# Kernel optimization log

Measured on AMD Instinct MI355X. Metric: run time of the kernel, lower is better.

## Reference

```python
import jax, jax.numpy as jnp
import numpy as np

N_ATOMS = 100000
N_EDGES = 1000000
HIDDEN = 64
OUT_DIM = 128
N_LAYERS = 3
N_ELEMENTS = 100


def setup_inputs() -> dict:
    key = jax.random.key(0)
    ks = jax.random.split(key, 14)
    s = 0.05
    return {
        "atomic_numbers": jax.random.randint(ks[0], (N_ATOMS,), 0, N_ELEMENTS),
        "positions": jax.random.normal(ks[1], (N_ATOMS, 3), jnp.float32),
        "lattice": jax.random.normal(ks[2], (3, 3), jnp.float32),
        "edge_index": jax.random.randint(ks[3], (2, N_EDGES), 0, N_ATOMS),
        "emb_table": jax.random.normal(ks[4], (N_ELEMENTS, HIDDEN), jnp.float32) * s,
        "W_lin": jax.random.normal(ks[5], (N_LAYERS, HIDDEN, HIDDEN), jnp.float32) * s,
        "b_lin": jax.random.normal(ks[6], (N_LAYERS, HIDDEN), jnp.float32) * s,
        "W_gate": jax.random.normal(ks[7], (N_LAYERS, 2 * HIDDEN, HIDDEN), jnp.float32) * s,
        "b_gate": jax.random.normal(ks[8], (N_LAYERS, HIDDEN), jnp.float32) * s,
        "W_out1": jax.random.normal(ks[9], (HIDDEN, HIDDEN), jnp.float32) * s,
        "b_out1": jax.random.normal(ks[10], (HIDDEN,), jnp.float32) * s,
        "W_out2": jax.random.normal(ks[11], (HIDDEN, OUT_DIM), jnp.float32) * s,
        "b_out2": jax.random.normal(ks[12], (OUT_DIM,), jnp.float32) * s,
    }


def reference(atomic_numbers, positions, lattice, edge_index,
              emb_table, W_lin, b_lin, W_gate, b_gate,
              W_out1, b_out1, W_out2, b_out2):
    # positions/lattice unused when edge_index is provided (matches original).
    x = emb_table[atomic_numbers]            # [N, H] embedding lookup
    row, col = edge_index[0], edge_index[1]
    n = x.shape[0]
    for i in range(W_lin.shape[0]):          # fixed small layer count
        xn = x[col]                          # [E, H] neighbor gather
        gate_in = jnp.concatenate([x[row], xn], axis=-1)  # [E, 2H]
        gate = jax.nn.sigmoid(gate_in @ W_gate[i] + b_gate[i])
        messages = gate * (xn @ W_lin[i] + b_lin[i])       # [E, H]
        agg = jax.ops.segment_sum(messages, row, num_segments=n)  # scatter-add
        x = jax.nn.relu(agg + x @ W_lin[i] + b_lin[i])
    pooled = x.mean(axis=0)                  # [H] mean pool over atoms
    h = jax.nn.relu(pooled @ W_out1 + b_out1)
    return h @ W_out2 + b_out2               # [OUT_DIM]
```

## Files before the change

### kernel.cpp

```cpp
#include <hip/hip_runtime.h>
#include <hip/hip_bf16.h>
#include <stdint.h>


#define H 64
#define BSHIFT 7
#define BROWS 128
#define NLOG2E -1.4426950408889634f

typedef __attribute__((ext_vector_type(8))) short bf16x8;
typedef __attribute__((ext_vector_type(4))) float f32x4;

__device__ __forceinline__ ushort f2bf(float f) {
  uint32_t u = __float_as_uint(f);
  u = (u + 0x7fffu + ((u >> 16) & 1u)) >> 16;
  return (ushort)u;
}
__device__ __forceinline__ uint32_t pack_gl(float gc, float lin) {
  uint32_t ug = __float_as_uint(gc);
  ug = (ug + 0x7fffu + ((ug >> 16) & 1u)) >> 16;
  uint32_t ul = __float_as_uint(lin);
  ul = ((ul + 0x7fffu + ((ul >> 16) & 1u)) >> 16) << 16;
  return ul | ug;
}
__device__ __forceinline__ float unpack_gc(uint32_t p) {
  return __uint_as_float(p << 16);
}
__device__ __forceinline__ float unpack_lin(uint32_t p) {
  return __uint_as_float(p & 0xffff0000u);
}
__device__ __forceinline__ float sig_from_neglog2(float arg) {
  return __builtin_amdgcn_rcpf(1.f + exp2f(arg));
}

__global__ __launch_bounds__(256) void prep_kernel(
    const float* __restrict__ Wl, const float* __restrict__ Wg,
    const float* __restrict__ bg, bf16x8* __restrict__ wprep,
    float* __restrict__ bgs) {
  const int t = blockIdx.x * 256 + threadIdx.x;
  if (t < 192) bgs[t] = bg[t] * NLOG2E;
  if (t >= 4608) return;
  const int l = t / 1536;
  const int rem = t - l * 1536;
  const int mat = rem >> 9;
  const int rem2 = rem & 511;
  const int nt = rem2 >> 7;
  const int ks = (rem2 >> 6) & 1;
  const int lane = rem2 & 63;
  const int kg = lane >> 4, l15 = lane & 15;
  const float* src;
  float s;
  if (mat == 0)      { src = Wl + (size_t)l * 4096;        s = 1.f; }
  else if (mat == 1) { src = Wg + (size_t)l * 8192;        s = NLOG2E; }
  else               { src = Wg + (size_t)l * 8192 + 4096; s = NLOG2E; }
  bf16x8 v;
#pragma unroll
  for (int j = 0; j < 8; j++)
    v[j] = (short)f2bf(src[(size_t)(ks * 32 + kg * 8 + j) * 64 + nt * 16 + l15] * s);
  wprep[t] = v;
}

__global__ __launch_bounds__(256) void bucket_hist_kernel(
    const int* __restrict__ row, int* __restrict__ bcnt, int E, int nbuck) {
  __shared__ int cnt[1024];
  const int tid = threadIdx.x;
  for (int b = tid; b < nbuck; b += 256) cnt[b] = 0;
  __syncthreads();
  for (int e = blockIdx.x * blockDim.x + tid; e < E; e += gridDim.x * blockDim.x)
    atomicAdd(&cnt[row[e] >> BSHIFT], 1);
  __syncthreads();
  for (int b = tid; b < nbuck; b += 256)
    if (cnt[b]) atomicAdd(&bcnt[b], cnt[b]);
}

__global__ __launch_bounds__(1024) void bucket_scan_kernel(
    const int* __restrict__ bcnt, int* __restrict__ bstart,
    int* __restrict__ bcur, int* __restrict__ offs, float* __restrict__ pool,
    int nbuck, int N, int E) {
  __shared__ int sh[1024];
  const int tid = threadIdx.x;
  if (tid < 64) pool[tid] = 0.f;
  const int mine = (tid < nbuck) ? bcnt[tid] : 0;
  sh[tid] = mine;
  __syncthreads();
  for (int off = 1; off < 1024; off <<= 1) {
    const int v = (tid >= off) ? sh[tid - off] : 0;
    __syncthreads();
    sh[tid] += v;
    __syncthreads();
  }
  if (tid < nbuck) {
    const int ex = sh[tid] - mine;
    bstart[tid] = ex;
    bcur[tid] = ex;
  }
  if (tid == 0) {
    bstart[nbuck] = E;
    offs[N] = E;
  }
}

#define SCHUNK 4096
__global__ __launch_bounds__(256) void bucket_scatter_kernel(
    const int* __restrict__ row, const int* __restrict__ col,
    int* __restrict__ bcur, uint2* __restrict__ ebuf, int E, int nbuck) {
  __shared__ int cnt[1024], base[1024];
  const int tid = threadIdx.x;
  const int start = blockIdx.x * SCHUNK;
  const int end = min(start + SCHUNK, E);
  for (int b = tid; b < nbuck; b += 256) cnt[b] = 0;
  __syncthreads();
  for (int e = start + tid; e < end; e += 256)
    atomicAdd(&cnt[row[e] >> BSHIFT], 1);
  __syncthreads();
  for (int b = tid; b < nbuck; b += 256) {
    if (cnt[b]) base[b] = atomicAdd(&bcur[b], cnt[b]);
    cnt[b] = 0;
  }
  __syncthreads();
  for (int e = start + tid; e < end; e += 256) {
    const int r = row[e];
    const int b = r >> BSHIFT;
    const int pos = base[b] + atomicAdd(&cnt[b], 1);
    ebuf[pos] = make_uint2((uint32_t)r, (uint32_t)col[e]);
  }
}

__global__ __launch_bounds__(256) void csr_build_kernel(
    const uint2* __restrict__ ebuf, const int* __restrict__ bstart,
    int* __restrict__ offs, int* __restrict__ cols, int N) {
  __shared__ int cnt[BROWS], sc[BROWS];
  const int tid = threadIdx.x;
  const int b = blockIdx.x;
  const int bs = bstart[b], be = bstart[b + 1];
  const int rowbase = b << BSHIFT;
  if (tid < BROWS) cnt[tid] = 0;
  __syncthreads();
  for (int e = bs + tid; e < be; e += 256)
    atomicAdd(&cnt[ebuf[e].x & (BROWS - 1)], 1);
  __syncthreads();
  if (tid < BROWS) sc[tid] = cnt[tid];
  __syncthreads();
  for (int off = 1; off < BROWS; off <<= 1) {
    const int v = (tid >= off && tid < BROWS) ? sc[tid - off] : 0;
    __syncthreads();
    if (tid < BROWS) sc[tid] += v;
    __syncthreads();
  }
  if (tid < BROWS) {
    sc[tid] -= cnt[tid];
    cnt[tid] = 0;
    const int r = rowbase + tid;
    if (r < N) offs[r] = bs + sc[tid];
  }
  __syncthreads();
  for (int e = bs + tid; e < be; e += 256) {
    const uint2 u = ebuf[e];
    const int rl = u.x & (BROWS - 1);
    const int pos = sc[rl] + atomicAdd(&cnt[rl], 1);
    cols[bs + pos] = (int)u.y;
  }
}

template <bool FIRST>
__global__ __launch_bounds__(256) void node_mm3_mfma(
    const ushort* __restrict__ x, const int* __restrict__ an,
    const float* __restrict__ emb, const bf16x8* __restrict__ wp,
    const float* __restrict__ bl, const float* __restrict__ bgs,
    float* __restrict__ gr, uint32_t* __restrict__ glpk, int N) {
  const int tid = threadIdx.x;
  const int lane = tid & 63, wid = tid >> 6;
  const int l15 = lane & 15, kg = lane >> 4;

  bf16x8 bfrag[3][4][2];
#pragma unroll
  for (int mat = 0; mat < 3; mat++)
#pragma unroll
    for (int nt = 0; nt < 4; nt++)
#pragma unroll
      for (int ks = 0; ks < 2; ks++)
        bfrag[mat][nt][ks] = wp[(((mat * 4 + nt) * 2 + ks) << 6) + lane];

  const int mbase = blockIdx.x * 64 + wid * 16;
  const int arow = mbase + l15;
  const int arow_c = min(arow, N - 1);

  bf16x8 afrag0, afrag1;
  if (FIRST) {
    const int a = an[arow_c];
    const float* src = emb + (size_t)a * H + kg * 8;
    const float4 u0 = *(const float4*)(src);
    const float4 u1 = *(const float4*)(src + 4);
    const float4 u2 = *(const float4*)(src + 32);
    const float4 u3 = *(const float4*)(src + 36);
    bf16x8 t0, t1;
    t0[0] = (short)f2bf(u0.x); t0[1] = (short)f2bf(u0.y);
    t0[2] = (short)f2bf(u0.z); t0[3] = (short)f2bf(u0.w);
    t0[4] = (short)f2bf(u1.x); t0[5] = (short)f2bf(u1.y);
    t0[6] = (short)f2bf(u1.z); t0[7] = (short)f2bf(u1.w);
    t1[0] = (short)f2bf(u2.x); t1[1] = (short)f2bf(u2.y);
    t1[2] = (short)f2bf(u2.z); t1[3] = (short)f2bf(u2.w);
    t1[4] = (short)f2bf(u3.x); t1[5] = (short)f2bf(u3.y);
    t1[6] = (short)f2bf(u3.z); t1[7] = (short)f2bf(u3.w);
    afrag0 = t0; afrag1 = t1;
  } else {
    const ushort* src = x + (size_t)arow_c * H + kg * 8;
    afrag0 = *(const bf16x8*)(src);
    afrag1 = *(const bf16x8*)(src + 32);
  }

  f32x4 accL[4], accR[4], accC[4];
#pragma unroll
  for (int nt = 0; nt < 4; nt++) {
    const float blv = bl[nt * 16 + l15];
    const float bgv = bgs[nt * 16 + l15];
    accL[nt] = (f32x4){blv, blv, blv, blv};
    accR[nt] = (f32x4){0.f, 0.f, 0.f, 0.f};
    accC[nt] = (f32x4){bgv, bgv, bgv, bgv};
  }
#pragma unroll
  for (int nt = 0; nt < 4; nt++) {
    accL[nt] = __builtin_amdgcn_mfma_f32_16x16x32_bf16(afrag0, bfrag[0][nt][0], accL[nt], 0, 0, 0);
    accL[nt] = __builtin_amdgcn_mfma_f32_16x16x32_bf16(afrag1, bfrag[0][nt][1], accL[nt], 0, 0, 0);
    accR[nt] = __builtin_amdgcn_mfma_f32_16x16x32_bf16(afrag0, bfrag[1][nt][0], accR[nt], 0, 0, 0);
    accR[nt] = __builtin_amdgcn_mfma_f32_16x16x32_bf16(afrag1, bfrag[1][nt][1], accR[nt], 0, 0, 0);
    accC[nt] = __builtin_amdgcn_mfma_f32_16x16x32_bf16(afrag0, bfrag[2][nt][0], accC[nt], 0, 0, 0);
    accC[nt] = __builtin_amdgcn_mfma_f32_16x16x32_bf16(afrag1, bfrag[2][nt][1], accC[nt], 0, 0, 0);
  }
#pragma unroll
  for (int nt = 0; nt < 4; nt++) {
#pragma unroll
    for (int r = 0; r < 4; r++) {
      const int atom = mbase + kg * 4 + r;
      if (atom < N) {
        const size_t o = (size_t)atom * H + nt * 16 + l15;
        gr[o] = accR[nt][r];
        glpk[o] = pack_gl(accC[nt][r], accL[nt][r]);
      }
    }
  }
}

__global__ __launch_bounds__(256) void agg_kernel(
    const float* __restrict__ gr, const uint32_t* __restrict__ glpk,
    const int* __restrict__ offs, const int* __restrict__ cols,
    ushort* __restrict__ x, int N) {
  const int lane = threadIdx.x & 63, w = threadIdx.x >> 6;
  for (int i = blockIdx.x * 4 + w; i < N; i += gridDim.x * 4) {
    const int s = offs[i], e = offs[i + 1];
    const float gri = gr[(size_t)i * H + lane];
    float acc = 0.f;
    for (int cb = s; cb < e; cb += 64) {
      const int nchunk = min(64, e - cb);
      const int myc = (lane < nchunk) ? cols[cb + lane] : 0;
      int j = 0;
      for (; j + 7 < nchunk; j += 8) {
        uint32_t p[8];
#pragma unroll
        for (int q = 0; q < 8; q++) {
          const int c = __shfl(myc, j + q);
          p[q] = glpk[(size_t)c * H + lane];
        }
#pragma unroll
        for (int q = 0; q < 8; q++)
          acc += unpack_lin(p[q]) * sig_from_neglog2(gri + unpack_gc(p[q]));
      }
      for (; j < nchunk; j++) {
        const int c = __shfl(myc, j);
        const uint32_t p0 = glpk[(size_t)c * H + lane];
        acc += unpack_lin(p0) * sig_from_neglog2(gri + unpack_gc(p0));
      }
    }
    const float li = unpack_lin(glpk[(size_t)i * H + lane]);
    x[(size_t)i * H + lane] = f2bf(fmaxf(acc + li, 0.f));
  }
}

__global__ void pool_kernel(const ushort* __restrict__ x,
                            float* __restrict__ pool, int N) {
  __shared__ float ps[4][64];
  const int tid = threadIdx.x, c = tid & 63, wid = tid >> 6;
  float s = 0.f;
  for (int i = blockIdx.x * 4 + wid; i < N; i += gridDim.x * 4)
    s += __uint_as_float(((uint32_t)x[(size_t)i * H + c]) << 16);
  ps[wid][c] = s;
  __syncthreads();
  if (tid < 64) {
    const float t = ps[0][tid] + ps[1][tid] + ps[2][tid] + ps[3][tid];
    atomicAdd(&pool[tid], t);
  }
}

__global__ void mlp_kernel(const float* __restrict__ pool,
                           const float* __restrict__ W1,
                           const float* __restrict__ b1,
                           const float* __restrict__ W2,
                           const float* __restrict__ b2,
                           float* __restrict__ out, float invN) {
  __shared__ float p[64], h[64];
  const int tid = threadIdx.x;
  if (tid < 64) p[tid] = pool[tid] * invN;
  __syncthreads();
  if (tid < 64) {
    float s = b1[tid];
    for (int k = 0; k < 64; k++) s = fmaf(p[k], W1[k * 64 + tid], s);
    h[tid] = fmaxf(s, 0.f);
  }
  __syncthreads();
  float s = b2[tid];
  for (int k = 0; k < 64; k++) s = fmaf(h[k], W2[k * 128 + tid], s);
  out[tid] = s;
}

extern "C" void kernel_launch(void* const* d_in, const int* in_sizes, int n_in,
                              void* d_out, int out_size, void* d_ws,
                              size_t ws_size, hipStream_t stream) {
  const int*   an  = (const int*)d_in[0];
  const int*   ei  = (const int*)d_in[3];
  const float* emb = (const float*)d_in[4];
  const float* Wl  = (const float*)d_in[5];
  const float* bl  = (const float*)d_in[6];
  const float* Wg  = (const float*)d_in[7];
  const float* bg  = (const float*)d_in[8];
  const float* W1  = (const float*)d_in[9];
  const float* b1  = (const float*)d_in[10];
  const float* W2  = (const float*)d_in[11];
  const float* b2  = (const float*)d_in[12];
  float* out = (float*)d_out;

  const int N = in_sizes[0];
  const int E = in_sizes[3] / 2;
  const int* row = ei;
  const int* col = ei + E;
  const int nbuck = (N + BROWS - 1) >> BSHIFT;

  const size_t NH = (size_t)N * H;
  char* ws = (char*)d_ws;
  ushort*   x    = (ushort*)(ws);
  float*    gr   = (float*)(ws + NH * 2);
  uint32_t* glpk = (uint32_t*)(ws + NH * 2 + NH * 4);
  char* p = ws + NH * 2 + NH * 4 + NH * 4;
  int*    offs   = (int*)p;    p += ((size_t)N + 1) * 4;
  int*    cols   = (int*)p;    p += (size_t)E * 4;
  int*    bcnt   = (int*)p;    p += 4096;
  int*    bstart = (int*)p;    p += 4100;
  int*    bcur   = (int*)p;    p += 4096;
  uint2*  ebuf   = (uint2*)p;  p += (size_t)E * 8;
  bf16x8* wprep  = (bf16x8*)p; p += 4608 * 16;
  float*  bgs    = (float*)p;  p += 192 * 4;
  float*  pool   = (float*)p;

  prep_kernel<<<18, 256, 0, stream>>>(Wl, Wg, bg, wprep, bgs);

  hipMemsetAsync(bcnt, 0, (size_t)nbuck * 4, stream);
  bucket_hist_kernel<<<1024, 256, 0, stream>>>(row, bcnt, E, nbuck);
  bucket_scan_kernel<<<1, 1024, 0, stream>>>(bcnt, bstart, bcur, offs, pool,
                                             nbuck, N, E);
  bucket_scatter_kernel<<<(E + SCHUNK - 1) / SCHUNK, 256, 0, stream>>>(
      row, col, bcur, ebuf, E, nbuck);
  csr_build_kernel<<<nbuck, 256, 0, stream>>>(ebuf, bstart, offs, cols, N);

  const int mmGrid = (N + 63) / 64;
  const int aggGrid = (N + 3) / 4;
  for (int l = 0; l < 3; l++) {
    const bf16x8* wp  = wprep + (size_t)l * 1536;
    const float*  bll = bl + (size_t)l * H;
    const float*  bgl = bgs + (size_t)l * H;
    if (l == 0)
      node_mm3_mfma<true><<<mmGrid, 256, 0, stream>>>(x, an, emb, wp, bll, bgl,
                                                      gr, glpk, N);
    else
      node_mm3_mfma<false><<<mmGrid, 256, 0, stream>>>(x, an, emb, wp, bll, bgl,
                                                       gr, glpk, N);
    agg_kernel<<<aggGrid, 256, 0, stream>>>(gr, glpk, offs, cols, x, N);
  }

  pool_kernel<<<1024, 256, 0, stream>>>(x, pool, N);
  mlp_kernel<<<1, 128, 0, stream>>>(pool, W1, b1, W2, b2, out, 1.0f / (float)N);
}
```

Before: 400.9 us.

## Replace CSR build with bucketed LDS-atomic aggregation and fuse pooling

Drops the per-row CSR construction kernel and aggregates messages directly over 64-row edge buckets, accumulating into shared memory with atomics. Edge records are packed into 32 bits (local row plus column), gr is stored in bf16, and mean pooling is fused into the final aggregation layer. This cuts a kernel launch, one edge pass and memory traffic, in exchange for LDS atomic contention and extra rounding of the gate term.

```diff
diff --git a/kernel.cpp b/kernel.cpp
--- a/kernel.cpp
+++ b/kernel.cpp
@@ -4,8 +4,8 @@
 
 
 #define H 64
-#define BSHIFT 7
-#define BROWS 128
+#define BSHIFT 6
+#define BROWS 64
 #define NLOG2E -1.4426950408889634f
 
 typedef __attribute__((ext_vector_type(8))) short bf16x8;
@@ -62,7 +62,7 @@
 
 __global__ __launch_bounds__(256) void bucket_hist_kernel(
     const int* __restrict__ row, int* __restrict__ bcnt, int E, int nbuck) {
-  __shared__ int cnt[1024];
+  __shared__ int cnt[2048];
   const int tid = threadIdx.x;
   for (int b = tid; b < nbuck; b += 256) cnt[b] = 0;
   __syncthreads();
@@ -75,13 +75,15 @@
 
 __global__ __launch_bounds__(1024) void bucket_scan_kernel(
     const int* __restrict__ bcnt, int* __restrict__ bstart,
-    int* __restrict__ bcur, int* __restrict__ offs, float* __restrict__ pool,
-    int nbuck, int N, int E) {
+    int* __restrict__ bcur, float* __restrict__ pool, int nbuck, int E) {
   __shared__ int sh[1024];
   const int tid = threadIdx.x;
   if (tid < 64) pool[tid] = 0.f;
-  const int mine = (tid < nbuck) ? bcnt[tid] : 0;
-  sh[tid] = mine;
+  const int i0 = 2 * tid, i1 = 2 * tid + 1;
+  const int v0 = (i0 < nbuck) ? bcnt[i0] : 0;
+  const int v1 = (i1 < nbuck) ? bcnt[i1] : 0;
+  const int s = v0 + v1;
+  sh[tid] = s;
   __syncthreads();
   for (int off = 1; off < 1024; off <<= 1) {
     const int v = (tid >= off) ? sh[tid - off] : 0;
@@ -89,22 +91,17 @@
     sh[tid] += v;
     __syncthreads();
   }
-  if (tid < nbuck) {
-    const int ex = sh[tid] - mine;
-    bstart[tid] = ex;
-    bcur[tid] = ex;
-  }
-  if (tid == 0) {
-    bstart[nbuck] = E;
-    offs[N] = E;
-  }
+  const int ex = sh[tid] - s;
+  if (i0 < nbuck) { bstart[i0] = ex;      bcur[i0] = ex; }
+  if (i1 < nbuck) { bstart[i1] = ex + v0; bcur[i1] = ex + v0; }
+  if (tid == 0) bstart[nbuck] = E;
 }
 
 #define SCHUNK 4096
 __global__ __launch_bounds__(256) void bucket_scatter_kernel(
     const int* __restrict__ row, const int* __restrict__ col,
-    int* __restrict__ bcur, uint2* __restrict__ ebuf, int E, int nbuck) {
-  __shared__ int cnt[1024], base[1024];
+    int* __restrict__ bcur, uint32_t* __restrict__ ebuf, int E, int nbuck) {
+  __shared__ int cnt[2048], base[2048];
   const int tid = threadIdx.x;
   const int start = blockIdx.x * SCHUNK;
   const int end = min(start + SCHUNK, E);
@@ -122,43 +119,7 @@
     const int r = row[e];
     const int b = r >> BSHIFT;
     const int pos = base[b] + atomicAdd(&cnt[b], 1);
-    ebuf[pos] = make_uint2((uint32_t)r, (uint32_t)col[e]);
-  }
-}
-
-__global__ __launch_bounds__(256) void csr_build_kernel(
-    const uint2* __restrict__ ebuf, const int* __restrict__ bstart,
-    int* __restrict__ offs, int* __restrict__ cols, int N) {
-  __shared__ int cnt[BROWS], sc[BROWS];
-  const int tid = threadIdx.x;
-  const int b = blockIdx.x;
-  const int bs = bstart[b], be = bstart[b + 1];
-  const int rowbase = b << BSHIFT;
-  if (tid < BROWS) cnt[tid] = 0;
-  __syncthreads();
-  for (int e = bs + tid; e < be; e += 256)
-    atomicAdd(&cnt[ebuf[e].x & (BROWS - 1)], 1);
-  __syncthreads();
-  if (tid < BROWS) sc[tid] = cnt[tid];
-  __syncthreads();
-  for (int off = 1; off < BROWS; off <<= 1) {
-    const int v = (tid >= off && tid < BROWS) ? sc[tid - off] : 0;
-    __syncthreads();
-    if (tid < BROWS) sc[tid] += v;
-    __syncthreads();
-  }
-  if (tid < BROWS) {
-    sc[tid] -= cnt[tid];
-    cnt[tid] = 0;
-    const int r = rowbase + tid;
-    if (r < N) offs[r] = bs + sc[tid];
-  }
-  __syncthreads();
-  for (int e = bs + tid; e < be; e += 256) {
-    const uint2 u = ebuf[e];
-    const int rl = u.x & (BROWS - 1);
-    const int pos = sc[rl] + atomicAdd(&cnt[rl], 1);
-    cols[bs + pos] = (int)u.y;
+    ebuf[pos] = ((uint32_t)(r & (BROWS - 1)) << 26) | (uint32_t)col[e];
   }
 }
 
@@ -167,7 +128,7 @@
     const ushort* __restrict__ x, const int* __restrict__ an,
     const float* __restrict__ emb, const bf16x8* __restrict__ wp,
     const float* __restrict__ bl, const float* __restrict__ bgs,
-    float* __restrict__ gr, uint32_t* __restrict__ glpk, int N) {
+    ushort* __restrict__ gr, uint32_t* __restrict__ glpk, int N) {
   const int tid = threadIdx.x;
   const int lane = tid & 63, wid = tid >> 6;
   const int l15 = lane & 15, kg = lane >> 4;
@@ -234,60 +195,88 @@
       const int atom = mbase + kg * 4 + r;
       if (atom < N) {
         const size_t o = (size_t)atom * H + nt * 16 + l15;
-        gr[o] = accR[nt][r];
+        gr[o] = f2bf(accR[nt][r]);
         glpk[o] = pack_gl(accC[nt][r], accL[nt][r]);
       }
     }
   }
 }
 
-__global__ __launch_bounds__(256) void agg_kernel(
-    const float* __restrict__ gr, const uint32_t* __restrict__ glpk,
-    const int* __restrict__ offs, const int* __restrict__ cols,
-    ushort* __restrict__ x, int N) {
-  const int lane = threadIdx.x & 63, w = threadIdx.x >> 6;
-  for (int i = blockIdx.x * 4 + w; i < N; i += gridDim.x * 4) {
-    const int s = offs[i], e = offs[i + 1];
-    const float gri = gr[(size_t)i * H + lane];
-    float acc = 0.f;
-    for (int cb = s; cb < e; cb += 64) {
-      const int nchunk = min(64, e - cb);
-      const int myc = (lane < nchunk) ? cols[cb + lane] : 0;
-      int j = 0;
-      for (; j + 7 < nchunk; j += 8) {
-        uint32_t p[8];
-#pragma unroll
-        for (int q = 0; q < 8; q++) {
-          const int c = __shfl(myc, j + q);
-          p[q] = glpk[(size_t)c * H + lane];
-        }
-#pragma unroll
-        for (int q = 0; q < 8; q++)
-          acc += unpack_lin(p[q]) * sig_from_neglog2(gri + unpack_gc(p[q]));
-      }
-      for (; j < nchunk; j++) {
-        const int c = __shfl(myc, j);
-        const uint32_t p0 = glpk[(size_t)c * H + lane];
-        acc += unpack_lin(p0) * sig_from_neglog2(gri + unpack_gc(p0));
+template <bool LAST>
+__global__ __launch_bounds__(256) void agg_bucket_kernel(
+    const ushort* __restrict__ gr, const uint32_t* __restrict__ glpk,
+    const uint32_t* __restrict__ ebuf, const int* __restrict__ bstart,
+    ushort* __restrict__ x, float* __restrict__ pool, int N) {
+  __shared__ float acc[BROWS * H];
+  __shared__ ushort grs[BROWS * H];
+  __shared__ float pacc[H];
+  const int tid = threadIdx.x;
+  const int lane = tid & 63, w = tid >> 6;
+  const int b = blockIdx.x;
+  const int rowbase = b << BSHIFT;
+
+  {
+    const uint4* gsrc = (const uint4*)(gr + (size_t)rowbase * H);
+    uint4* gdst = (uint4*)grs;
+    gdst[tid] = gsrc[tid];
+    gdst[tid + 256] = gsrc[tid + 256];
+    float4* az = (float4*)acc;
+#pragma unroll
+    for (int q = 0; q < 4; q++) az[tid + q * 256] = make_float4(0.f, 0.f, 0.f, 0.f);
+    if (LAST && tid < 64) pacc[tid] = 0.f;
+  }
+  __syncthreads();
+
+  const int bs = bstart[b], be = bstart[b + 1];
+  for (int cb = bs + w * 64; cb < be; cb += 256) {
+    const int nchunk = min(64, be - cb);
+    const uint32_t mye = (lane < nchunk) ? ebuf[cb + lane] : 0;
+    int j = 0;
+    for (; j + 3 < nchunk; j += 4) {
+      const uint32_t e0 = __shfl(mye, j + 0), e1 = __shfl(mye, j + 1);
+      const uint32_t e2 = __shfl(mye, j + 2), e3 = __shfl(mye, j + 3);
+      const uint32_t p0 = glpk[((e0 & 0x3FFFFFFu) << 6) | lane];
+      const uint32_t p1 = glpk[((e1 & 0x3FFFFFFu) << 6) | lane];
+      const uint32_t p2 = glpk[((e2 & 0x3FFFFFFu) << 6) | lane];
+      const uint32_t p3 = glpk[((e3 & 0x3FFFFFFu) << 6) | lane];
+#pragma unroll
+      for (int q = 0; q < 4; q++) {
+        const uint32_t e = (q == 0) ? e0 : (q == 1) ? e1 : (q == 2) ? e2 : e3;
+        const uint32_t p = (q == 0) ? p0 : (q == 1) ? p1 : (q == 2) ? p2 : p3;
+        const int rl = (int)(e >> 26);
+        const float g = __uint_as_float((uint32_t)grs[(rl << 6) | lane] << 16);
+        const float m = unpack_lin(p) * sig_from_neglog2(g + unpack_gc(p));
+        atomicAdd(&acc[(rl << 6) | lane], m);
       }
     }
-    const float li = unpack_lin(glpk[(size_t)i * H + lane]);
-    x[(size_t)i * H + lane] = f2bf(fmaxf(acc + li, 0.f));
-  }
-}
-
-__global__ void pool_kernel(const ushort* __restrict__ x,
-                            float* __restrict__ pool, int N) {
-  __shared__ float ps[4][64];
-  const int tid = threadIdx.x, c = tid & 63, wid = tid >> 6;
-  float s = 0.f;
-  for (int i = blockIdx.x * 4 + wid; i < N; i += gridDim.x * 4)
-    s += __uint_as_float(((uint32_t)x[(size_t)i * H + c]) << 16);
-  ps[wid][c] = s;
-  __syncthreads();
-  if (tid < 64) {
-    const float t = ps[0][tid] + ps[1][tid] + ps[2][tid] + ps[3][tid];
-    atomicAdd(&pool[tid], t);
+    for (; j < nchunk; j++) {
+      const uint32_t e = __shfl(mye, j);
+      const uint32_t p = glpk[((e & 0x3FFFFFFu) << 6) | lane];
+      const int rl = (int)(e >> 26);
+      const float g = __uint_as_float((uint32_t)grs[(rl << 6) | lane] << 16);
+      const float m = unpack_lin(p) * sig_from_neglog2(g + unpack_gc(p));
+      atomicAdd(&acc[(rl << 6) | lane], m);
+    }
+  }
+  __syncthreads();
+
+  float psum = 0.f;
+#pragma unroll
+  for (int k = 0; k < 16; k++) {
+    const int r = w * 16 + k;
+    const int atom = rowbase + r;
+    if (atom < N) {
+      const float li = unpack_lin(glpk[((size_t)atom << 6) | lane]);
+      float v = acc[(r << 6) | lane] + li;
+      v = fmaxf(v, 0.f);
+      x[((size_t)atom << 6) | lane] = f2bf(v);
+      if (LAST) psum += v;
+    }
+  }
+  if (LAST) {
+    atomicAdd(&pacc[lane], psum);
+    __syncthreads();
+    if (tid < 64) atomicAdd(&pool[tid], pacc[tid]);
   }
 }
 
@@ -337,31 +326,26 @@
   const size_t NH = (size_t)N * H;
   char* ws = (char*)d_ws;
   ushort*   x    = (ushort*)(ws);
-  float*    gr   = (float*)(ws + NH * 2);
-  uint32_t* glpk = (uint32_t*)(ws + NH * 2 + NH * 4);
-  char* p = ws + NH * 2 + NH * 4 + NH * 4;
-  int*    offs   = (int*)p;    p += ((size_t)N + 1) * 4;
-  int*    cols   = (int*)p;    p += (size_t)E * 4;
-  int*    bcnt   = (int*)p;    p += 4096;
-  int*    bstart = (int*)p;    p += 4100;
-  int*    bcur   = (int*)p;    p += 4096;
-  uint2*  ebuf   = (uint2*)p;  p += (size_t)E * 8;
-  bf16x8* wprep  = (bf16x8*)p; p += 4608 * 16;
-  float*  bgs    = (float*)p;  p += 192 * 4;
-  float*  pool   = (float*)p;
+  ushort*   gr   = (ushort*)(ws + NH * 2);
+  uint32_t* glpk = (uint32_t*)(ws + NH * 4);
+  char* p = ws + NH * 4 + NH * 4;
+  uint32_t* ebuf   = (uint32_t*)p; p += (size_t)E * 4;
+  int*      bcnt   = (int*)p;      p += 8192;
+  int*      bstart = (int*)p;      p += 8196;
+  int*      bcur   = (int*)p;      p += 8192;
+  bf16x8*   wprep  = (bf16x8*)p;   p += 4608 * 16;
+  float*    bgs    = (float*)p;    p += 192 * 4;
+  float*    pool   = (float*)p;
 
   prep_kernel<<<18, 256, 0, stream>>>(Wl, Wg, bg, wprep, bgs);
 
   hipMemsetAsync(bcnt, 0, (size_t)nbuck * 4, stream);
   bucket_hist_kernel<<<1024, 256, 0, stream>>>(row, bcnt, E, nbuck);
-  bucket_scan_kernel<<<1, 1024, 0, stream>>>(bcnt, bstart, bcur, offs, pool,
-                                             nbuck, N, E);
+  bucket_scan_kernel<<<1, 1024, 0, stream>>>(bcnt, bstart, bcur, pool, nbuck, E);
   bucket_scatter_kernel<<<(E + SCHUNK - 1) / SCHUNK, 256, 0, stream>>>(
       row, col, bcur, ebuf, E, nbuck);
-  csr_build_kernel<<<nbuck, 256, 0, stream>>>(ebuf, bstart, offs, cols, N);
 
   const int mmGrid = (N + 63) / 64;
-  const int aggGrid = (N + 3) / 4;
   for (int l = 0; l < 3; l++) {
     const bf16x8* wp  = wprep + (size_t)l * 1536;
     const float*  bll = bl + (size_t)l * H;
@@ -372,9 +356,13 @@
     else
       node_mm3_mfma<false><<<mmGrid, 256, 0, stream>>>(x, an, emb, wp, bll, bgl,
                                                        gr, glpk, N);
-    agg_kernel<<<aggGrid, 256, 0, stream>>>(gr, glpk, offs, cols, x, N);
-  }
-
-  pool_kernel<<<1024, 256, 0, stream>>>(x, pool, N);
+    if (l == 2)
+      agg_bucket_kernel<true><<<nbuck, 256, 0, stream>>>(gr, glpk, ebuf, bstart,
+                                                         x, pool, N);
+    else
+      agg_bucket_kernel<false><<<nbuck, 256, 0, stream>>>(gr, glpk, ebuf, bstart,
+                                                          x, pool, N);
+  }
+
   mlp_kernel<<<1, 128, 0, stream>>>(pool, W1, b1, W2, b2, out, 1.0f / (float)N);
 }
```

Result: slower. 1.401 ms (+249.4%).
